# Kernel optimization log

Measured on AMD Instinct MI355X. Metric: run time of the kernel, lower is better.

Reference implementation:

```python
import jax, jax.numpy as jnp
import numpy as np

SCALE_FACTOR = 0.25  # init kwarg


def _fps_indices(pos_b, M):
    """Batched farthest point sampling.
    pos_b: [B, P, 3]. Returns local indices [B, M].
    Deterministic start at point 0 of each cloud (torch_cluster's
    random_start replaced by fixed start for reproducibility).
    """
    B, P, _ = pos_b.shape
    # squared distance of every point to the start point -> initial min-dist
    min_d0 = jnp.sum((pos_b - pos_b[:, :1]) ** 2, axis=-1)  # [B, P]

    def step(min_d, _):
        sel = jnp.argmax(min_d, axis=1)                              # [B]
        p = jnp.take_along_axis(pos_b, sel[:, None, None], axis=1)   # [B,1,3]
        d = jnp.sum((pos_b - p) ** 2, axis=-1)                       # [B,P]
        return jnp.minimum(min_d, d), sel

    _, sels = jax.lax.scan(step, min_d0, None, length=M - 1)  # [M-1, B]
    first = jnp.zeros((B, 1), dtype=sels.dtype)
    return jnp.concatenate([first, sels.T], axis=1)  # [B, M]


def setup_inputs() -> dict:
    key = jax.random.key(0)
    k1, k2 = jax.random.split(key)
    B, P, F = 16, 16384, 128
    N = B * P
    x = jax.random.normal(k1, (N, F), dtype=jnp.float32)
    pos = jax.random.normal(k2, (N, 3), dtype=jnp.float32) * 10.0
    batch = jnp.repeat(jnp.arange(B, dtype=jnp.int32), P)  # sorted cloud ids
    return {"x": x, "pos": pos, "batch": batch}


def reference(x, pos, batch):
    B = int(batch[-1]) + 1
    N = pos.shape[0]
    P = N // B                      # equal-sized clouds (batch is sorted repeats)
    M = int(SCALE_FACTOR * P)       # points kept per cloud
    pos_b = pos.reshape(B, P, 3)
    idx = _fps_indices(pos_b, M)                              # [B, M] local
    gidx = (idx + jnp.arange(B, dtype=idx.dtype)[:, None] * P).reshape(-1)
    return x[gidx], pos[gidx], batch[gidx]
```

## Files before the change

### kernel.cpp

```cpp
#include <hip/hip_runtime.h>

#define FPS_T 1024
#define FPS_K 16
#define NW    (FPS_T / 64)
#define NCELL 512

__device__ __forceinline__ float sqd_f32dag(float ax, float ay, float az,
                                            float bx, float by, float bz) {
    const float dx = __fsub_rn(ax, bx);
    const float dy = __fsub_rn(ay, by);
    const float dz = __fsub_rn(az, bz);
    float acc = __fmul_rn(dy, dy);
    acc = __builtin_fmaf(dx, dx, acc);
    acc = __builtin_fmaf(dz, dz, acc);
    return acc;
}

__global__ __launch_bounds__(1024) void preprocess_kernel(const float* __restrict__ pos,
                                                          float* __restrict__ pxw,
                                                          float* __restrict__ pyw,
                                                          float* __restrict__ pzw,
                                                          unsigned short* __restrict__ tlw,
                                                          int P) {
    const int b = blockIdx.x, t = threadIdx.x;
    const float* posb = pos + (size_t)b * P * 3;
    float* PX = pxw + (size_t)b * P;
    float* PY = pyw + (size_t)b * P;
    float* PZ = pzw + (size_t)b * P;
    unsigned short* TL = tlw + (size_t)b * P;

    __shared__ unsigned hist[NCELL];
    __shared__ unsigned scanb[NCELL];
    __shared__ float s_red[NW][8];

    float x[FPS_K], y[FPS_K], z[FPS_K];
    float lx = 1e30f, ly = 1e30f, lz = 1e30f, hx = -1e30f, hy = -1e30f, hz = -1e30f;
#pragma unroll
    for (int k = 0; k < FPS_K; ++k) {
        const int p = k * FPS_T + t;
        x[k] = posb[p * 3 + 0]; y[k] = posb[p * 3 + 1]; z[k] = posb[p * 3 + 2];
        lx = fminf(lx, x[k]); hx = fmaxf(hx, x[k]);
        ly = fminf(ly, y[k]); hy = fmaxf(hy, y[k]);
        lz = fminf(lz, z[k]); hz = fmaxf(hz, z[k]);
    }
#pragma unroll
    for (int off = 32; off >= 1; off >>= 1) {
        lx = fminf(lx, __shfl_xor(lx, off, 64)); hx = fmaxf(hx, __shfl_xor(hx, off, 64));
        ly = fminf(ly, __shfl_xor(ly, off, 64)); hy = fmaxf(hy, __shfl_xor(hy, off, 64));
        lz = fminf(lz, __shfl_xor(lz, off, 64)); hz = fmaxf(hz, __shfl_xor(hz, off, 64));
    }
    if ((t & 63) == 0) {
        const int w = t >> 6;
        s_red[w][0] = lx; s_red[w][1] = ly; s_red[w][2] = lz;
        s_red[w][3] = hx; s_red[w][4] = hy; s_red[w][5] = hz;
    }
    if (t < NCELL) hist[t] = 0;
    __syncthreads();
    lx = s_red[0][0]; ly = s_red[0][1]; lz = s_red[0][2];
    hx = s_red[0][3]; hy = s_red[0][4]; hz = s_red[0][5];
#pragma unroll
    for (int w = 1; w < NW; ++w) {
        lx = fminf(lx, s_red[w][0]); ly = fminf(ly, s_red[w][1]); lz = fminf(lz, s_red[w][2]);
        hx = fmaxf(hx, s_red[w][3]); hy = fmaxf(hy, s_red[w][4]); hz = fmaxf(hz, s_red[w][5]);
    }
    const float ivx = 8.0f / fmaxf(hx - lx, 1e-20f);
    const float ivy = 8.0f / fmaxf(hy - ly, 1e-20f);
    const float ivz = 8.0f / fmaxf(hz - lz, 1e-20f);

    int cid[FPS_K];
#pragma unroll
    for (int k = 0; k < FPS_K; ++k) {
        int cx = (int)((x[k] - lx) * ivx); cx = cx < 0 ? 0 : (cx > 7 ? 7 : cx);
        int cy = (int)((y[k] - ly) * ivy); cy = cy < 0 ? 0 : (cy > 7 ? 7 : cy);
        int cz = (int)((z[k] - lz) * ivz); cz = cz < 0 ? 0 : (cz > 7 ? 7 : cz);
        cid[k] = (cx << 6) | (cy << 3) | cz;
        atomicAdd(&hist[cid[k]], 1u);
    }
    __syncthreads();
    if (t < NCELL) scanb[t] = hist[t];
    __syncthreads();
    for (int off = 1; off < NCELL; off <<= 1) {
        unsigned add = 0;
        if (t < NCELL && t >= off) add = scanb[t - off];
        __syncthreads();
        if (t < NCELL) scanb[t] += add;
        __syncthreads();
    }
    if (t < NCELL) hist[t] = scanb[t] - hist[t];
    __syncthreads();
#pragma unroll
    for (int k = 0; k < FPS_K; ++k) {
        const int p = k * FPS_T + t;
        const unsigned dst = atomicAdd(&hist[cid[k]], 1u);
        PX[dst] = x[k]; PY[dst] = y[k]; PZ[dst] = z[k];
        TL[dst] = (unsigned short)(16383 - p);
    }
}

__global__ __launch_bounds__(1024) void fps_kernel(const float* __restrict__ pos,
                                                   const float* __restrict__ pxw,
                                                   const float* __restrict__ pyw,
                                                   const float* __restrict__ pzw,
                                                   const unsigned short* __restrict__ tlw,
                                                   int* __restrict__ idx_out,
                                                   int P, int M) {
#pragma clang fp contract(off)
    const int b = blockIdx.x, t = threadIdx.x;
    const float* posb = pos + (size_t)b * P * 3;
    const float* PX = pxw + (size_t)b * P;
    const float* PY = pyw + (size_t)b * P;
    const float* PZ = pzw + (size_t)b * P;
    const unsigned* TL = (const unsigned*)(tlw + (size_t)b * P);

    __shared__ unsigned long long s_key[2][NW];

    float px[FPS_K], py[FPS_K], pz[FPS_K], md[FPS_K];
    unsigned tlp[FPS_K / 2];
    const int sp0 = t * FPS_K;
    {
        const float4* a = (const float4*)(PX + sp0);
        const float4* c = (const float4*)(PY + sp0);
        const float4* e = (const float4*)(PZ + sp0);
#pragma unroll
        for (int j = 0; j < FPS_K / 4; ++j) {
            const float4 v = a[j]; px[4*j] = v.x; px[4*j+1] = v.y; px[4*j+2] = v.z; px[4*j+3] = v.w;
            const float4 w = c[j]; py[4*j] = w.x; py[4*j+1] = w.y; py[4*j+2] = w.z; py[4*j+3] = w.w;
            const float4 u = e[j]; pz[4*j] = u.x; pz[4*j+1] = u.y; pz[4*j+2] = u.z; pz[4*j+3] = u.w;
        }
        const uint4 q0 = ((const uint4*)TL)[t * 2];
        const uint4 q1 = ((const uint4*)TL)[t * 2 + 1];
        tlp[0] = q0.x; tlp[1] = q0.y; tlp[2] = q0.z; tlp[3] = q0.w;
        tlp[4] = q1.x; tlp[5] = q1.y; tlp[6] = q1.z; tlp[7] = q1.w;
    }
    float blx = px[0], bhx = px[0], bly = py[0], bhy = py[0], blz = pz[0], bhz = pz[0];
#pragma unroll
    for (int k = 1; k < FPS_K; ++k) {
        blx = fminf(blx, px[k]); bhx = fmaxf(bhx, px[k]);
        bly = fminf(bly, py[k]); bhy = fmaxf(bhy, py[k]);
        blz = fminf(blz, pz[k]); bhz = fmaxf(bhz, pz[k]);
    }
#pragma unroll
    for (int k = 0; k < FPS_K; ++k) md[k] = __builtin_inff();
    if (t == 0) idx_out[(size_t)b * M] = 0;

    float sx = posb[0], sy = posb[1], sz = posb[2];
    unsigned long long ckey = 0ull, wkey = 0ull;
    float thresh = __builtin_inff();

    for (int m = 1; m < M; ++m) {
        const float cx = fminf(fmaxf(sx, blx), bhx);
        const float cy = fminf(fmaxf(sy, bly), bhy);
        const float cz = fminf(fmaxf(sz, blz), bhz);
        const float bb = sqd_f32dag(cx, cy, cz, sx, sy, sz);
        const bool active = !(bb >= thresh);
        if (__ballot(active) != 0ull) {
            if (active) {
                unsigned long long bk = 0ull;
#pragma unroll
                for (int k = 0; k < FPS_K; ++k) {
                    const float d  = sqd_f32dag(px[k], py[k], pz[k], sx, sy, sz);
                    const float nm = fminf(md[k], d);
                    md[k] = nm;
                    const unsigned tor = (tlp[k >> 1] >> ((k & 1) * 16)) & 0xFFFFu;
                    const unsigned long long kk =
                        ((unsigned long long)__float_as_uint(nm) << 32)
                        | (unsigned long long)((tor << 14) | (unsigned)(sp0 + k));
                    if (kk > bk) bk = kk;
                }
                ckey = bk;
                thresh = __uint_as_float((unsigned)(bk >> 32)) * 1.00006104f;
            }
            unsigned long long key = ckey;
#pragma unroll
            for (int off = 32; off >= 1; off >>= 1) {
                const unsigned long long o = __shfl_xor(key, off, 64);
                if (o > key) key = o;
            }
            wkey = key;
        }
        const int buf = m & 1;
        if ((t & 63) == 0) s_key[buf][t >> 6] = wkey;
        __syncthreads();
        unsigned long long g = s_key[buf][t & (NW - 1)];
#pragma unroll
        for (int off = NW / 2; off >= 1; off >>= 1) {
            const unsigned long long o = __shfl_xor(g, off, NW);
            if (o > g) g = o;
        }
        if (t == 0) idx_out[(size_t)b * M + m] = 16383 - (int)((g >> 14) & 0x3FFF);
        const int spos = __builtin_amdgcn_readfirstlane((int)(g & 0x3FFF));
        sx = PX[spos]; sy = PY[spos]; sz = PZ[spos];
    }
}

__global__ __launch_bounds__(256) void gather_kernel(const float* __restrict__ x,
                                                     const float* __restrict__ pos,
                                                     const int* __restrict__ idx,
                                                     float* __restrict__ out,
                                                     int P, int M, int F, int BM) {
    const int r    = blockIdx.x * 8 + (threadIdx.x >> 5);
    const int lane = threadIdx.x & 31;
    if (r >= BM) return;
    const int b  = r / M;
    const int li = idx[r];
    const size_t g = (size_t)b * P + li;

    const float4* xr   = reinterpret_cast<const float4*>(x + g * (size_t)F);
    float4*       orow = reinterpret_cast<float4*>(out + (size_t)r * F);
    orow[lane] = xr[lane];

    const size_t pos_base   = (size_t)BM * F;
    const size_t batch_base = pos_base + (size_t)BM * 3;
    if (lane < 3)  out[pos_base + (size_t)r * 3 + lane] = pos[g * 3 + lane];
    if (lane == 3) out[batch_base + r] = (float)b;
}

extern "C" void kernel_launch(void* const* d_in, const int* in_sizes, int n_in,
                              void* d_out, int out_size, void* d_ws, size_t ws_size,
                              hipStream_t stream) {
    const float* x   = (const float*)d_in[0];
    const float* pos = (const float*)d_in[1];
    const int N = in_sizes[2];
    const int F = in_sizes[0] / N;
    const int B = 16;
    const int P = N / B;
    const int M = P / 4;
    const int BM = B * M;
    const int PP = B * P;

    int* idx_ws = (int*)d_ws;

    float* out_f = (float*)d_out;
    const int scratch_elems = 3 * PP + PP / 2;
    float* pxw = out_f + (out_size - scratch_elems);
    float* pyw = pxw + PP;
    float* pzw = pyw + PP;
    unsigned short* tlw = (unsigned short*)(pzw + PP);

    preprocess_kernel<<<B, FPS_T, 0, stream>>>(pos, pxw, pyw, pzw, tlw, P);
    fps_kernel<<<B, FPS_T, 0, stream>>>(pos, pxw, pyw, pzw, tlw, idx_ws, P, M);
    gather_kernel<<<(BM + 7) / 8, 256, 0, stream>>>(x, pos, idx_ws, (float*)d_out, P, M, F, BM);
}
```

Before: 5.447 ms.

## Select two FPS points per iteration when the runner-up is provably next

The FPS loop now tracks the top-2 candidate keys per thread, wave and block. When the second-best point's distance to the best point is at least its own current min-distance, it is provably the next FPS choice, so both points are emitted in one iteration and both distance updates are applied together. This can roughly halve the number of block-wide barriers and reductions on the serial path, at the cost of twice the shuffle traffic and extra compares per iteration. Point storage also changes to an interleaved float4 (x, y, z, tie-key) layout, so each selected point is fetched with one vector load instead of three scalar loads.

```diff
diff --git a/kernel.cpp b/kernel.cpp
--- a/kernel.cpp
+++ b/kernel.cpp
@@ -16,18 +16,21 @@
     return acc;
 }
 
+__device__ __forceinline__ void p2_merge(unsigned long long& a1, unsigned long long& a2,
+                                         unsigned long long b1, unsigned long long b2) {
+    const unsigned long long hi = a1 > b1 ? a1 : b1;
+    const unsigned long long lo = a1 > b1 ? b1 : a1;
+    const unsigned long long m2 = a2 > b2 ? a2 : b2;
+    a1 = hi;
+    a2 = lo > m2 ? lo : m2;
+}
+
 __global__ __launch_bounds__(1024) void preprocess_kernel(const float* __restrict__ pos,
-                                                          float* __restrict__ pxw,
-                                                          float* __restrict__ pyw,
-                                                          float* __restrict__ pzw,
-                                                          unsigned short* __restrict__ tlw,
+                                                          float4* __restrict__ pxyz,
                                                           int P) {
     const int b = blockIdx.x, t = threadIdx.x;
     const float* posb = pos + (size_t)b * P * 3;
-    float* PX = pxw + (size_t)b * P;
-    float* PY = pyw + (size_t)b * P;
-    float* PZ = pzw + (size_t)b * P;
-    unsigned short* TL = tlw + (size_t)b * P;
+    float4* PB = pxyz + (size_t)b * P;
 
     __shared__ unsigned hist[NCELL];
     __shared__ unsigned scanb[NCELL];
@@ -92,45 +95,31 @@
     for (int k = 0; k < FPS_K; ++k) {
         const int p = k * FPS_T + t;
         const unsigned dst = atomicAdd(&hist[cid[k]], 1u);
-        PX[dst] = x[k]; PY[dst] = y[k]; PZ[dst] = z[k];
-        TL[dst] = (unsigned short)(16383 - p);
+        PB[dst] = make_float4(x[k], y[k], z[k], __uint_as_float((unsigned)(16383 - p)));
     }
 }
 
 __global__ __launch_bounds__(1024) void fps_kernel(const float* __restrict__ pos,
-                                                   const float* __restrict__ pxw,
-                                                   const float* __restrict__ pyw,
-                                                   const float* __restrict__ pzw,
-                                                   const unsigned short* __restrict__ tlw,
+                                                   const float4* __restrict__ pxyz,
                                                    int* __restrict__ idx_out,
                                                    int P, int M) {
 #pragma clang fp contract(off)
     const int b = blockIdx.x, t = threadIdx.x;
     const float* posb = pos + (size_t)b * P * 3;
-    const float* PX = pxw + (size_t)b * P;
-    const float* PY = pyw + (size_t)b * P;
-    const float* PZ = pzw + (size_t)b * P;
-    const unsigned* TL = (const unsigned*)(tlw + (size_t)b * P);
-
-    __shared__ unsigned long long s_key[2][NW];
+    const float4* PB = pxyz + (size_t)b * P;
+
+    __shared__ ulonglong2 s_pair[2][NW];
 
     float px[FPS_K], py[FPS_K], pz[FPS_K], md[FPS_K];
     unsigned tlp[FPS_K / 2];
     const int sp0 = t * FPS_K;
-    {
-        const float4* a = (const float4*)(PX + sp0);
-        const float4* c = (const float4*)(PY + sp0);
-        const float4* e = (const float4*)(PZ + sp0);
-#pragma unroll
-        for (int j = 0; j < FPS_K / 4; ++j) {
-            const float4 v = a[j]; px[4*j] = v.x; px[4*j+1] = v.y; px[4*j+2] = v.z; px[4*j+3] = v.w;
-            const float4 w = c[j]; py[4*j] = w.x; py[4*j+1] = w.y; py[4*j+2] = w.z; py[4*j+3] = w.w;
-            const float4 u = e[j]; pz[4*j] = u.x; pz[4*j+1] = u.y; pz[4*j+2] = u.z; pz[4*j+3] = u.w;
-        }
-        const uint4 q0 = ((const uint4*)TL)[t * 2];
-        const uint4 q1 = ((const uint4*)TL)[t * 2 + 1];
-        tlp[0] = q0.x; tlp[1] = q0.y; tlp[2] = q0.z; tlp[3] = q0.w;
-        tlp[4] = q1.x; tlp[5] = q1.y; tlp[6] = q1.z; tlp[7] = q1.w;
+#pragma unroll
+    for (int k = 0; k < FPS_K; ++k) {
+        const float4 v = PB[sp0 + k];
+        px[k] = v.x; py[k] = v.y; pz[k] = v.z;
+        const unsigned tor = __float_as_uint(v.w);
+        if ((k & 1) == 0) tlp[k >> 1] = tor; else tlp[k >> 1] |= tor << 16;
+        md[k] = __builtin_inff();
     }
     float blx = px[0], bhx = px[0], bly = py[0], bhy = py[0], blz = pz[0], bhz = pz[0];
 #pragma unroll
@@ -139,57 +128,95 @@
         bly = fminf(bly, py[k]); bhy = fmaxf(bhy, py[k]);
         blz = fminf(blz, pz[k]); bhz = fmaxf(bhz, pz[k]);
     }
-#pragma unroll
-    for (int k = 0; k < FPS_K; ++k) md[k] = __builtin_inff();
     if (t == 0) idx_out[(size_t)b * M] = 0;
 
-    float sx = posb[0], sy = posb[1], sz = posb[2];
-    unsigned long long ckey = 0ull, wkey = 0ull;
+    float s1x = posb[0], s1y = posb[1], s1z = posb[2];
+    float s2x = 0.f, s2y = 0.f, s2z = 0.f;
+    bool have2 = false;
+    unsigned long long ck1 = 0ull, ck2 = 0ull, wk1 = 0ull, wk2 = 0ull;
     float thresh = __builtin_inff();
-
-    for (int m = 1; m < M; ++m) {
-        const float cx = fminf(fmaxf(sx, blx), bhx);
-        const float cy = fminf(fmaxf(sy, bly), bhy);
-        const float cz = fminf(fmaxf(sz, blz), bhz);
-        const float bb = sqd_f32dag(cx, cy, cz, sx, sy, sz);
-        const bool active = !(bb >= thresh);
-        if (__ballot(active) != 0ull) {
-            if (active) {
-                unsigned long long bk = 0ull;
-#pragma unroll
-                for (int k = 0; k < FPS_K; ++k) {
-                    const float d  = sqd_f32dag(px[k], py[k], pz[k], sx, sy, sz);
-                    const float nm = fminf(md[k], d);
-                    md[k] = nm;
-                    const unsigned tor = (tlp[k >> 1] >> ((k & 1) * 16)) & 0xFFFFu;
-                    const unsigned long long kk =
-                        ((unsigned long long)__float_as_uint(nm) << 32)
-                        | (unsigned long long)((tor << 14) | (unsigned)(sp0 + k));
-                    if (kk > bk) bk = kk;
+    int m = 1, buf = 0;
+
+    while (m < M) {
+        float cx = fminf(fmaxf(s1x, blx), bhx);
+        float cy = fminf(fmaxf(s1y, bly), bhy);
+        float cz = fminf(fmaxf(s1z, blz), bhz);
+        bool act = sqd_f32dag(cx, cy, cz, s1x, s1y, s1z) < thresh;
+        if (have2) {
+            cx = fminf(fmaxf(s2x, blx), bhx);
+            cy = fminf(fmaxf(s2y, bly), bhy);
+            cz = fminf(fmaxf(s2z, blz), bhz);
+            act = act || (sqd_f32dag(cx, cy, cz, s2x, s2y, s2z) < thresh);
+        }
+        if (__ballot(act) != 0ull) {
+            if (act) {
+                unsigned long long bk1 = 0ull, bk2 = 0ull;
+                if (have2) {
+#pragma unroll
+                    for (int k = 0; k < FPS_K; ++k) {
+                        const float d1 = sqd_f32dag(px[k], py[k], pz[k], s1x, s1y, s1z);
+                        const float d2 = sqd_f32dag(px[k], py[k], pz[k], s2x, s2y, s2z);
+                        const float nm = fminf(fminf(md[k], d1), d2);
+                        md[k] = nm;
+                        const unsigned tor = (tlp[k >> 1] >> ((k & 1) * 16)) & 0xFFFFu;
+                        const unsigned long long kk =
+                            ((unsigned long long)__float_as_uint(nm) << 32)
+                            | (unsigned long long)((tor << 14) | (unsigned)(sp0 + k));
+                        if (kk > bk1) { bk2 = bk1; bk1 = kk; }
+                        else if (kk > bk2) { bk2 = kk; }
+                    }
+                } else {
+#pragma unroll
+                    for (int k = 0; k < FPS_K; ++k) {
+                        const float d1 = sqd_f32dag(px[k], py[k], pz[k], s1x, s1y, s1z);
+                        const float nm = fminf(md[k], d1);
+                        md[k] = nm;
+                        const unsigned tor = (tlp[k >> 1] >> ((k & 1) * 16)) & 0xFFFFu;
+                        const unsigned long long kk =
+                            ((unsigned long long)__float_as_uint(nm) << 32)
+                            | (unsigned long long)((tor << 14) | (unsigned)(sp0 + k));
+                        if (kk > bk1) { bk2 = bk1; bk1 = kk; }
+                        else if (kk > bk2) { bk2 = kk; }
+                    }
                 }
-                ckey = bk;
-                thresh = __uint_as_float((unsigned)(bk >> 32)) * 1.00006104f;
+                ck1 = bk1; ck2 = bk2;
+                thresh = __uint_as_float((unsigned)(bk1 >> 32)) * 1.00006104f;
             }
-            unsigned long long key = ckey;
+            unsigned long long k1 = ck1, k2 = ck2;
 #pragma unroll
             for (int off = 32; off >= 1; off >>= 1) {
-                const unsigned long long o = __shfl_xor(key, off, 64);
-                if (o > key) key = o;
+                const unsigned long long o1 = __shfl_xor(k1, off, 64);
+                const unsigned long long o2 = __shfl_xor(k2, off, 64);
+                p2_merge(k1, k2, o1, o2);
             }
-            wkey = key;
-        }
-        const int buf = m & 1;
-        if ((t & 63) == 0) s_key[buf][t >> 6] = wkey;
+            wk1 = k1; wk2 = k2;
+        }
+        if ((t & 63) == 0) s_pair[buf][t >> 6] = make_ulonglong2(wk1, wk2);
         __syncthreads();
-        unsigned long long g = s_key[buf][t & (NW - 1)];
+        const ulonglong2 pr = s_pair[buf][t & (NW - 1)];
+        unsigned long long g1 = pr.x, g2 = pr.y;
 #pragma unroll
         for (int off = NW / 2; off >= 1; off >>= 1) {
-            const unsigned long long o = __shfl_xor(g, off, NW);
-            if (o > g) g = o;
-        }
-        if (t == 0) idx_out[(size_t)b * M + m] = 16383 - (int)((g >> 14) & 0x3FFF);
-        const int spos = __builtin_amdgcn_readfirstlane((int)(g & 0x3FFF));
-        sx = PX[spos]; sy = PY[spos]; sz = PZ[spos];
+            const unsigned long long o1 = __shfl_xor(g1, off, NW);
+            const unsigned long long o2 = __shfl_xor(g2, off, NW);
+            p2_merge(g1, g2, o1, o2);
+        }
+        const int s1i = __builtin_amdgcn_readfirstlane((int)(g1 & 0x3FFFu));
+        const int s2i = __builtin_amdgcn_readfirstlane((int)(g2 & 0x3FFFu));
+        const float4 w1 = PB[s1i];
+        const float4 w2 = PB[s2i];
+        const float v2val = __uint_as_float((unsigned)(g2 >> 32));
+        const float d21 = sqd_f32dag(w2.x, w2.y, w2.z, w1.x, w1.y, w1.z);
+        const bool paired = (d21 >= v2val) && (v2val > 0.0f) && (m + 1 < M);
+        if (t == 0) {
+            idx_out[(size_t)b * M + m] = 16383 - (int)((g1 >> 14) & 0x3FFFu);
+            if (paired) idx_out[(size_t)b * M + m + 1] = 16383 - (int)((g2 >> 14) & 0x3FFFu);
+        }
+        s1x = w1.x; s1y = w1.y; s1z = w1.z;
+        s2x = w2.x; s2y = w2.y; s2z = w2.z;
+        have2 = paired;
+        m += paired ? 2 : 1;
+        buf ^= 1;
     }
 }
 
@@ -231,13 +258,9 @@
     int* idx_ws = (int*)d_ws;
 
     float* out_f = (float*)d_out;
-    const int scratch_elems = 3 * PP + PP / 2;
-    float* pxw = out_f + (out_size - scratch_elems);
-    float* pyw = pxw + PP;
-    float* pzw = pyw + PP;
-    unsigned short* tlw = (unsigned short*)(pzw + PP);
-
-    preprocess_kernel<<<B, FPS_T, 0, stream>>>(pos, pxw, pyw, pzw, tlw, P);
-    fps_kernel<<<B, FPS_T, 0, stream>>>(pos, pxw, pyw, pzw, tlw, idx_ws, P, M);
+    float4* pxyz = (float4*)(out_f + (out_size - 4 * PP));
+
+    preprocess_kernel<<<B, FPS_T, 0, stream>>>(pos, pxyz, P);
+    fps_kernel<<<B, FPS_T, 0, stream>>>(pos, pxyz, idx_ws, P, M);
     gather_kernel<<<(BM + 7) / 8, 256, 0, stream>>>(x, pos, idx_ws, (float*)d_out, P, M, F, BM);
 }
```

Measured after the change: 10.81 ms. 98.4% more time.

## Pack sorted points as float4 and broadcast winner position via shared memory

Applied to the files above, without the earlier changes.

Preprocessing now writes each sorted point as one float4 holding xyz plus the original index. The FPS loop keeps the winning point's coordinates next to its key and publishes them per wave to shared memory, so the next centre is read from LDS instead of a dependent global load each iteration. The wave reduction now does a float max plus a ballot and only falls back to a 64-bit key reduction when values tie. Side effects: scratch grows to four floats per point, and the idx_out write rotates across waves.

```diff
diff --git a/kernel.cpp b/kernel.cpp
--- a/kernel.cpp
+++ b/kernel.cpp
@@ -17,17 +17,11 @@
 }
 
 __global__ __launch_bounds__(1024) void preprocess_kernel(const float* __restrict__ pos,
-                                                          float* __restrict__ pxw,
-                                                          float* __restrict__ pyw,
-                                                          float* __restrict__ pzw,
-                                                          unsigned short* __restrict__ tlw,
+                                                          float4* __restrict__ pxyz,
                                                           int P) {
     const int b = blockIdx.x, t = threadIdx.x;
     const float* posb = pos + (size_t)b * P * 3;
-    float* PX = pxw + (size_t)b * P;
-    float* PY = pyw + (size_t)b * P;
-    float* PZ = pzw + (size_t)b * P;
-    unsigned short* TL = tlw + (size_t)b * P;
+    float4* PB = pxyz + (size_t)b * P;
 
     __shared__ unsigned hist[NCELL];
     __shared__ unsigned scanb[NCELL];
@@ -92,45 +86,33 @@
     for (int k = 0; k < FPS_K; ++k) {
         const int p = k * FPS_T + t;
         const unsigned dst = atomicAdd(&hist[cid[k]], 1u);
-        PX[dst] = x[k]; PY[dst] = y[k]; PZ[dst] = z[k];
-        TL[dst] = (unsigned short)(16383 - p);
+        PB[dst] = make_float4(x[k], y[k], z[k], __uint_as_float((unsigned)(16383 - p)));
     }
 }
 
 __global__ __launch_bounds__(1024) void fps_kernel(const float* __restrict__ pos,
-                                                   const float* __restrict__ pxw,
-                                                   const float* __restrict__ pyw,
-                                                   const float* __restrict__ pzw,
-                                                   const unsigned short* __restrict__ tlw,
+                                                   const float4* __restrict__ pxyz,
                                                    int* __restrict__ idx_out,
                                                    int P, int M) {
 #pragma clang fp contract(off)
     const int b = blockIdx.x, t = threadIdx.x;
+    const int lane = t & 63, w = t >> 6;
     const float* posb = pos + (size_t)b * P * 3;
-    const float* PX = pxw + (size_t)b * P;
-    const float* PY = pyw + (size_t)b * P;
-    const float* PZ = pzw + (size_t)b * P;
-    const unsigned* TL = (const unsigned*)(tlw + (size_t)b * P);
-
-    __shared__ unsigned long long s_key[2][NW];
+    const float4* PB = pxyz + (size_t)b * P;
+
+    __shared__ float    s_val[2][NW];
+    __shared__ unsigned s_pay[2][NW];
+    __shared__ float4   s_wpos[2][NW];
 
     float px[FPS_K], py[FPS_K], pz[FPS_K], md[FPS_K];
-    unsigned tlp[FPS_K / 2];
+    unsigned pay[FPS_K];
     const int sp0 = t * FPS_K;
-    {
-        const float4* a = (const float4*)(PX + sp0);
-        const float4* c = (const float4*)(PY + sp0);
-        const float4* e = (const float4*)(PZ + sp0);
-#pragma unroll
-        for (int j = 0; j < FPS_K / 4; ++j) {
-            const float4 v = a[j]; px[4*j] = v.x; px[4*j+1] = v.y; px[4*j+2] = v.z; px[4*j+3] = v.w;
-            const float4 w = c[j]; py[4*j] = w.x; py[4*j+1] = w.y; py[4*j+2] = w.z; py[4*j+3] = w.w;
-            const float4 u = e[j]; pz[4*j] = u.x; pz[4*j+1] = u.y; pz[4*j+2] = u.z; pz[4*j+3] = u.w;
-        }
-        const uint4 q0 = ((const uint4*)TL)[t * 2];
-        const uint4 q1 = ((const uint4*)TL)[t * 2 + 1];
-        tlp[0] = q0.x; tlp[1] = q0.y; tlp[2] = q0.z; tlp[3] = q0.w;
-        tlp[4] = q1.x; tlp[5] = q1.y; tlp[6] = q1.z; tlp[7] = q1.w;
+#pragma unroll
+    for (int k = 0; k < FPS_K; ++k) {
+        const float4 v = PB[sp0 + k];
+        px[k] = v.x; py[k] = v.y; pz[k] = v.z;
+        pay[k] = (__float_as_uint(v.w) << 14) | (unsigned)(sp0 + k);
+        md[k] = __builtin_inff();
     }
     float blx = px[0], bhx = px[0], bly = py[0], bhy = py[0], blz = pz[0], bhz = pz[0];
 #pragma unroll
@@ -139,57 +121,72 @@
         bly = fminf(bly, py[k]); bhy = fmaxf(bhy, py[k]);
         blz = fminf(blz, pz[k]); bhz = fmaxf(bhz, pz[k]);
     }
-#pragma unroll
-    for (int k = 0; k < FPS_K; ++k) md[k] = __builtin_inff();
     if (t == 0) idx_out[(size_t)b * M] = 0;
 
+    float cval = -1.0f; unsigned cpay = 0u;
+    float cbx = 0.f, cby = 0.f, cbz = 0.f;
+    bool  owner = false;
+    float thresh = __builtin_inff();
     float sx = posb[0], sy = posb[1], sz = posb[2];
-    unsigned long long ckey = 0ull, wkey = 0ull;
-    float thresh = __builtin_inff();
 
     for (int m = 1; m < M; ++m) {
+        const int buf = m & 1;
         const float cx = fminf(fmaxf(sx, blx), bhx);
         const float cy = fminf(fmaxf(sy, bly), bhy);
         const float cz = fminf(fmaxf(sz, blz), bhz);
         const float bb = sqd_f32dag(cx, cy, cz, sx, sy, sz);
-        const bool active = !(bb >= thresh);
+        const bool active = bb < thresh;
         if (__ballot(active) != 0ull) {
             if (active) {
-                unsigned long long bk = 0ull;
+                float bval = -1.0f; unsigned bpay = 0u;
+                float bx = 0.f, by = 0.f, bz = 0.f;
 #pragma unroll
                 for (int k = 0; k < FPS_K; ++k) {
                     const float d  = sqd_f32dag(px[k], py[k], pz[k], sx, sy, sz);
                     const float nm = fminf(md[k], d);
                     md[k] = nm;
-                    const unsigned tor = (tlp[k >> 1] >> ((k & 1) * 16)) & 0xFFFFu;
-                    const unsigned long long kk =
-                        ((unsigned long long)__float_as_uint(nm) << 32)
-                        | (unsigned long long)((tor << 14) | (unsigned)(sp0 + k));
-                    if (kk > bk) bk = kk;
+                    const bool better = (nm > bval) || (nm == bval && pay[k] > bpay);
+                    if (better) { bval = nm; bpay = pay[k]; bx = px[k]; by = py[k]; bz = pz[k]; }
                 }
-                ckey = bk;
-                thresh = __uint_as_float((unsigned)(bk >> 32)) * 1.00006104f;
+                cval = bval; cpay = bpay; cbx = bx; cby = by; cbz = bz;
+                thresh = bval * 1.00006104f;
             }
-            unsigned long long key = ckey;
-#pragma unroll
-            for (int off = 32; off >= 1; off >>= 1) {
-                const unsigned long long o = __shfl_xor(key, off, 64);
-                if (o > key) key = o;
+            float wv = cval;
+#pragma unroll
+            for (int off = 32; off >= 1; off >>= 1)
+                wv = fmaxf(wv, __shfl_xor(wv, off, 64));
+            const unsigned long long mask = __ballot(cval == wv);
+            if (__popcll(mask) == 1) {
+                owner = (mask >> lane) & 1ull;
+            } else {
+                unsigned long long kk = ((unsigned long long)__float_as_uint(cval) << 32) | cpay;
+                unsigned long long wm = kk;
+#pragma unroll
+                for (int off = 32; off >= 1; off >>= 1) {
+                    const unsigned long long o = __shfl_xor(wm, off, 64);
+                    if (o > wm) wm = o;
+                }
+                owner = (kk == wm);
             }
-            wkey = key;
         }
-        const int buf = m & 1;
-        if ((t & 63) == 0) s_key[buf][t >> 6] = wkey;
+        if (owner) {
+            s_val[buf][w]  = cval;
+            s_pay[buf][w]  = cpay;
+            s_wpos[buf][w] = make_float4(cbx, cby, cbz, 0.0f);
+        }
         __syncthreads();
-        unsigned long long g = s_key[buf][t & (NW - 1)];
+        const int sl = lane & (NW - 1);
+        unsigned long long g = ((unsigned long long)__float_as_uint(s_val[buf][sl]) << 32)
+                             | s_pay[buf][sl];
 #pragma unroll
         for (int off = NW / 2; off >= 1; off >>= 1) {
             const unsigned long long o = __shfl_xor(g, off, NW);
             if (o > g) g = o;
         }
-        if (t == 0) idx_out[(size_t)b * M + m] = 16383 - (int)((g >> 14) & 0x3FFF);
-        const int spos = __builtin_amdgcn_readfirstlane((int)(g & 0x3FFF));
-        sx = PX[spos]; sy = PY[spos]; sz = PZ[spos];
+        const unsigned gp = (unsigned)g;
+        if (t == ((m & 15) << 6)) idx_out[(size_t)b * M + m] = 16383 - (int)((gp >> 14) & 0x3FFFu);
+        const float4 wp = s_wpos[buf][(gp & 0x3FFFu) >> 10];
+        sx = wp.x; sy = wp.y; sz = wp.z;
     }
 }
 
@@ -231,13 +228,9 @@
     int* idx_ws = (int*)d_ws;
 
     float* out_f = (float*)d_out;
-    const int scratch_elems = 3 * PP + PP / 2;
-    float* pxw = out_f + (out_size - scratch_elems);
-    float* pyw = pxw + PP;
-    float* pzw = pyw + PP;
-    unsigned short* tlw = (unsigned short*)(pzw + PP);
-
-    preprocess_kernel<<<B, FPS_T, 0, stream>>>(pos, pxw, pyw, pzw, tlw, P);
-    fps_kernel<<<B, FPS_T, 0, stream>>>(pos, pxw, pyw, pzw, tlw, idx_ws, P, M);
+    float4* pxyz = (float4*)(out_f + (out_size - 4 * PP));
+
+    preprocess_kernel<<<B, FPS_T, 0, stream>>>(pos, pxyz, P);
+    fps_kernel<<<B, FPS_T, 0, stream>>>(pos, pxyz, idx_ws, P, M);
     gather_kernel<<<(BM + 7) / 8, 256, 0, stream>>>(x, pos, idx_ws, (float*)d_out, P, M, F, BM);
 }
```

Result: slower. 8.061 ms (+48.0%).
